# Kernel tuning notes

Measured on AMD Instinct MI355X. Metric: run time of the kernel, lower is better.

Reference implementation:

```python
import jax, jax.numpy as jnp
import numpy as np

K = 9          # kernel_size
PAD = K // 2   # 'same' padding, stride 1
SIGMA = 1.0
EPS = 1e-5     # BatchNorm eps

def _windows(a):
    # a: (B, C, L) -> (B, C, K, L); zero-padded sliding windows (== F.unfold semantics)
    L = a.shape[-1]
    ap = jnp.pad(a, ((0, 0), (0, 0), (PAD, PAD)))
    return jnp.stack([ap[:, :, k:k + L] for k in range(K)], axis=2)

def setup_inputs() -> dict:
    key = jax.random.key(0)
    ks = jax.random.split(key, 4)
    B, Cin, Cout, L = 8, 256, 256, 16384
    x = jax.random.normal(ks[0], (B, Cin, L), jnp.float32)
    coords = jax.random.uniform(ks[1], (B, 3, L), jnp.float32)
    conv_w = jax.random.normal(ks[2], (Cout, Cin, K), jnp.float32) * np.float32(1.0 / np.sqrt(Cin * K))
    conv_b = jnp.zeros((Cout,), jnp.float32)
    gamma = jnp.ones((Cout,), jnp.float32)
    beta = jnp.zeros((Cout,), jnp.float32)
    return {"x": x, "coords": coords, "conv_w": conv_w, "conv_b": conv_b, "gamma": gamma, "beta": beta}

def reference(x, coords, conv_w, conv_b, gamma, beta):
    # --- WeightedConv1D: Gaussian coordinate weights on each unfolded window element ---
    cw = _windows(coords)                                      # (B, 3, K, L)
    d2 = jnp.sum((cw - coords[:, :, None, :]) ** 2, axis=1)    # (B, K, L) squared dist to window center
    w = jnp.exp(-d2 / (2.0 * SIGMA ** 2))                      # (B, K, L) Gaussian weights
    xw = _windows(x) * w[:, None, :, :]                        # (B, Cin, K, L) weighted windows
    y = jnp.einsum('bckl,ock->bol', xw, conv_w) + conv_b[None, :, None]  # (B, Cout, L)
    # --- BatchNorm1d (training-mode batch statistics, biased variance) + ReLU ---
    mu = jnp.mean(y, axis=(0, 2), keepdims=True)
    var = jnp.var(y, axis=(0, 2), keepdims=True)
    yhat = (y - mu) * jax.lax.rsqrt(var + EPS)
    out = jax.nn.relu(yhat * gamma[None, :, None] + beta[None, :, None])
    # Dropout with drop=0.0 is the identity.
    return out
```

## Files before the change

kernel.cpp:

```cpp
#include <hip/hip_runtime.h>
#include <hip/hip_bf16.h>


typedef float        f32x4  __attribute__((ext_vector_type(4)));
typedef short        bf16x8 __attribute__((ext_vector_type(8)));
typedef unsigned int u32x4  __attribute__((ext_vector_type(4)));

#define LLEN 16384

__device__ __forceinline__ unsigned short bf16bits(float a) {
  return __builtin_bit_cast(unsigned short, __float2bfloat16(a));
}
__device__ __forceinline__ unsigned packbf(float a, float b) {
  return (unsigned)bf16bits(a) | ((unsigned)bf16bits(b) << 16);
}

__global__ void k_prep(const float* __restrict__ cw,
                       unsigned short* __restrict__ Aperm,
                       float* __restrict__ sums) {
  const int idx = blockIdx.x * 256 + threadIdx.x;
  if (idx < 512) sums[idx] = 0.0f;
  const int o   = idx / 2304;
  const int rem = idx - o * 2304;
  const int c   = rem / 9;
  const int kk  = rem - c * 9;
  Aperm[((size_t)kk * 256 + o) * 256 + c] = bf16bits(cw[idx]);
}

__global__ void k_w(const float* __restrict__ coords, float* __restrict__ wbuf) {
  const int gidx = blockIdx.x * 256 + threadIdx.x;
  const int b = gidx >> 14, l = gidx & (LLEN - 1);
  const float* cb = coords + (size_t)b * 3 * LLEN;
  const float c0 = cb[l], c1 = cb[LLEN + l], c2v = cb[2 * LLEN + l];
#pragma unroll
  for (int kk = 0; kk < 9; ++kk) {
    const int lc = l + kk - 4;
    float a0 = 0.f, a1 = 0.f, a2 = 0.f;
    if (lc >= 0 && lc < LLEN) { a0 = cb[lc]; a1 = cb[LLEN + lc]; a2 = cb[2 * LLEN + lc]; }
    const float d0 = a0 - c0, d1 = a1 - c1, d2 = a2 - c2v;
    wbuf[(((size_t)(b * 9 + kk)) << 14) + l] = __expf(-0.5f * (d0 * d0 + d1 * d1 + d2 * d2));
  }
}

__global__ __launch_bounds__(512, 2) void k_gemm(
    const float* __restrict__ x, const float* __restrict__ wbuf,
    const unsigned short* __restrict__ Aperm, const float* __restrict__ convb,
    float* __restrict__ y, float* __restrict__ sums) {
  __shared__ __align__(16) unsigned short Ash[256][72];
  __shared__ __align__(16) unsigned short Xsh[264][72];

  const int tid  = threadIdx.x;
  const int lane = tid & 63, wv = tid >> 6;
  const int wm = wv >> 2, wn = wv & 3;
  const int hi = lane >> 4, lo16 = lane & 15;
  const int b  = blockIdx.x >> 6, lt = blockIdx.x & 63;
  const int l0 = lt << 8;

  f32x4 acc[8][4];
#pragma unroll
  for (int i = 0; i < 8; ++i)
#pragma unroll
    for (int j = 0; j < 4; ++j) acc[i][j] = f32x4{0.f, 0.f, 0.f, 0.f};

  const int arow  = tid >> 3;
  const int acol8 = (tid & 7) * 8;
  const int nbase = wn * 64 + lo16;

  u32x4 ar[4];
  float wl[4], wln[4];

#pragma unroll
  for (int p = 0; p < 4; ++p)
    ar[p] = *reinterpret_cast<const u32x4*>(
        Aperm + ((size_t)(p * 64 + arow)) * 256 + acol8);
#pragma unroll
  for (int nt = 0; nt < 4; ++nt)
    wl[nt] = wbuf[((size_t)(b * 9) << 14) + l0 + nbase + nt * 16];

#pragma unroll 1
  for (int cc = 0; cc < 4; ++cc) {
    __syncthreads();
    {
      const int c = tid >> 3, rg = tid & 7;
      const float* xrow = x + ((size_t)(b * 256 + cc * 64 + c)) * LLEN;
#pragma unroll 1
      for (int grp = rg; grp < 66; grp += 8) {
        const int lx = l0 - 4 + grp * 4;
        f32x4 v;
        if (lx >= 0 && lx <= LLEN - 4) {
          v = *reinterpret_cast<const f32x4*>(xrow + lx);
        } else {
#pragma unroll
          for (int q = 0; q < 4; ++q) {
            const int lq = lx + q;
            v[q] = (lq >= 0 && lq < LLEN) ? xrow[lq] : 0.f;
          }
        }
#pragma unroll
        for (int q = 0; q < 4; ++q) Xsh[grp * 4 + q][c] = bf16bits(v[q]);
      }
    }
#pragma unroll 1
    for (int kk = 0; kk < 9; ++kk) {
      if (kk) __syncthreads();
#pragma unroll
      for (int p = 0; p < 4; ++p)
        *reinterpret_cast<u32x4*>(reinterpret_cast<char*>(&Ash[0][0]) +
                                  (p * 64 + arow) * 144 + acol8 * 2) = ar[p];
      int nkk = kk + 1, ncc = cc;
      if (nkk == 9) { nkk = 0; ++ncc; if (ncc == 4) { ncc = 3; nkk = 8; } }
#pragma unroll
      for (int p = 0; p < 4; ++p)
        ar[p] = *reinterpret_cast<const u32x4*>(
            Aperm + ((size_t)nkk * 256 + p * 64 + arow) * 256 + ncc * 64 + acol8);
#pragma unroll
      for (int nt = 0; nt < 4; ++nt)
        wln[nt] = wbuf[((size_t)(b * 9 + nkk) << 14) + l0 + nbase + nt * 16];
      __syncthreads();
#pragma unroll
      for (int kb = 0; kb < 2; ++kb) {
        bf16x8 bfrag[4];
#pragma unroll
        for (int nt = 0; nt < 4; ++nt) {
          const int r = nbase + nt * 16 + kk;
          const u32x4 xr = *reinterpret_cast<const u32x4*>(
              reinterpret_cast<const char*>(&Xsh[0][0]) + r * 144 + kb * 64 + hi * 16);
          const float wv2 = wl[nt];
          u32x4 o4;
#pragma unroll
          for (int q = 0; q < 4; ++q) {
            const unsigned u = xr[q];
            const float flo = __builtin_bit_cast(float, u << 16) * wv2;
            const float fhi = __builtin_bit_cast(float, u & 0xffff0000u) * wv2;
            o4[q] = packbf(flo, fhi);
          }
          bfrag[nt] = __builtin_bit_cast(bf16x8, o4);
        }
#pragma unroll
        for (int mt = 0; mt < 8; ++mt) {
          const int orow = wm * 128 + mt * 16 + lo16;
          const bf16x8 af = *reinterpret_cast<const bf16x8*>(
              reinterpret_cast<const char*>(&Ash[0][0]) + orow * 144 + kb * 64 + hi * 16);
#pragma unroll
          for (int nt = 0; nt < 4; ++nt)
            acc[mt][nt] = __builtin_amdgcn_mfma_f32_16x16x32_bf16(af, bfrag[nt],
                                                                  acc[mt][nt], 0, 0, 0);
        }
      }
#pragma unroll
      for (int nt = 0; nt < 4; ++nt) wl[nt] = wln[nt];
    }
  }

  __syncthreads();
  float* red = reinterpret_cast<float*>(&Ash[0][0]);
  red[tid] = 0.0f;
  __syncthreads();
#pragma unroll
  for (int mt = 0; mt < 8; ++mt) {
#pragma unroll
    for (int v = 0; v < 4; ++v) {
      const int o = wm * 128 + mt * 16 + hi * 4 + v;
      const float cb = convb[o];
      float s = 0.f, s2 = 0.f;
#pragma unroll
      for (int nt = 0; nt < 4; ++nt) {
        const int l = l0 + nbase + nt * 16;
        const float yv = acc[mt][nt][v] + cb;
        y[(((size_t)b * 256 + o) << 14) + l] = yv;
        s += yv; s2 += yv * yv;
      }
#pragma unroll
      for (int d = 1; d < 16; d <<= 1) { s += __shfl_xor(s, d); s2 += __shfl_xor(s2, d); }
      if (lo16 == 0) { atomicAdd(&red[o], s); atomicAdd(&red[o + 256], s2); }
    }
  }
  __syncthreads();
  atomicAdd(&sums[tid], red[tid]);
}

__global__ void k_norm(float* __restrict__ y, const float* __restrict__ sums,
                       const float* __restrict__ gamma, const float* __restrict__ beta) {
  const size_t i0 = ((size_t)blockIdx.x * 256 + threadIdx.x) * 8;
  const int o = (int)((i0 >> 14) & 255);
  const float n = 131072.f;
  const float mu = sums[o] / n;
  float var = sums[256 + o] / n - mu * mu;
  var = fmaxf(var, 0.f);
  const float sc = rsqrtf(var + 1e-5f) * gamma[o];
  const float bb = beta[o] - mu * sc;
  f32x4 v0 = *reinterpret_cast<const f32x4*>(y + i0);
  f32x4 v1 = *reinterpret_cast<const f32x4*>(y + i0 + 4);
#pragma unroll
  for (int i = 0; i < 4; ++i) {
    v0[i] = fmaxf(v0[i] * sc + bb, 0.f);
    v1[i] = fmaxf(v1[i] * sc + bb, 0.f);
  }
  *reinterpret_cast<f32x4*>(y + i0) = v0;
  *reinterpret_cast<f32x4*>(y + i0 + 4) = v1;
}

extern "C" void kernel_launch(void* const* d_in, const int* in_sizes, int n_in,
                              void* d_out, int out_size, void* d_ws, size_t ws_size,
                              hipStream_t stream) {
  const float* x      = (const float*)d_in[0];
  const float* coords = (const float*)d_in[1];
  const float* conv_w = (const float*)d_in[2];
  const float* conv_b = (const float*)d_in[3];
  const float* gamma  = (const float*)d_in[4];
  const float* beta   = (const float*)d_in[5];
  float* out = (float*)d_out;

  float* sums = (float*)d_ws;
  float* wbuf = (float*)((char*)d_ws + 4096);
  unsigned short* Aperm =
      (unsigned short*)((char*)d_ws + 4096 + (size_t)8 * 9 * LLEN * 4);

  k_prep<<<2304, 256, 0, stream>>>(conv_w, Aperm, sums);
  k_w<<<512, 256, 0, stream>>>(coords, wbuf);
  k_gemm<<<512, 512, 0, stream>>>(x, wbuf, Aperm, conv_b, out, sums);
  k_norm<<<16384, 256, 0, stream>>>(out, sums, gamma, beta);
}
```

Before: 273.5 us.

## Load GEMM weight fragments directly from global memory and prefetch x chunks in registers

Drops the shared-memory staging of the conv-weight tile, so each wave reads its A fragments straight from the permuted bf16 weight buffer in global memory (L2-resident). This removes the per-tap A store and two syncs per inner iteration. The next x channel chunk is prefetched into registers as packed bf16 while the current chunk is computed. Float-to-bf16 packing now uses the hardware v_cvt_pk_bf16_f32 instruction. In exchange it adds redundant global and L2 traffic for weights across waves, with load latency exposed inside the MFMA loop, plus more register pressure.

```diff
diff --git a/kernel.cpp b/kernel.cpp
--- a/kernel.cpp
+++ b/kernel.cpp
@@ -4,6 +4,7 @@
 
 typedef float        f32x4  __attribute__((ext_vector_type(4)));
 typedef short        bf16x8 __attribute__((ext_vector_type(8)));
+typedef unsigned int u32x2  __attribute__((ext_vector_type(2)));
 typedef unsigned int u32x4  __attribute__((ext_vector_type(4)));
 
 #define LLEN 16384
@@ -11,8 +12,10 @@
 __device__ __forceinline__ unsigned short bf16bits(float a) {
   return __builtin_bit_cast(unsigned short, __float2bfloat16(a));
 }
-__device__ __forceinline__ unsigned packbf(float a, float b) {
-  return (unsigned)bf16bits(a) | ((unsigned)bf16bits(b) << 16);
+__device__ __forceinline__ unsigned cvt_pk_bf16(float lo, float hi) {
+  unsigned r;
+  asm("v_cvt_pk_bf16_f32 %0, %1, %2" : "=v"(r) : "v"(lo), "v"(hi));
+  return r;
 }
 
 __global__ void k_prep(const float* __restrict__ cw,
@@ -46,7 +49,6 @@
     const float* __restrict__ x, const float* __restrict__ wbuf,
     const unsigned short* __restrict__ Aperm, const float* __restrict__ convb,
     float* __restrict__ y, float* __restrict__ sums) {
-  __shared__ __align__(16) unsigned short Ash[256][72];
   __shared__ __align__(16) unsigned short Xsh[264][72];
 
   const int tid  = threadIdx.x;
@@ -55,6 +57,7 @@
   const int hi = lane >> 4, lo16 = lane & 15;
   const int b  = blockIdx.x >> 6, lt = blockIdx.x & 63;
   const int l0 = lt << 8;
+  const int nbase = wn * 64 + lo16;
 
   f32x4 acc[8][4];
 #pragma unroll
@@ -62,98 +65,89 @@
 #pragma unroll
     for (int j = 0; j < 4; ++j) acc[i][j] = f32x4{0.f, 0.f, 0.f, 0.f};
 
-  const int arow  = tid >> 3;
-  const int acol8 = (tid & 7) * 8;
-  const int nbase = wn * 64 + lo16;
-
-  u32x4 ar[4];
-  float wl[4], wln[4];
-
-#pragma unroll
-  for (int p = 0; p < 4; ++p)
-    ar[p] = *reinterpret_cast<const u32x4*>(
-        Aperm + ((size_t)(p * 64 + arow)) * 256 + acol8);
-#pragma unroll
-  for (int nt = 0; nt < 4; ++nt)
-    wl[nt] = wbuf[((size_t)(b * 9) << 14) + l0 + nbase + nt * 16];
-
+  const int c = tid >> 3, rg = tid & 7;
+  u32x2 xp[9];
+
+  auto loadx = [&](int cc) {
+    const float* xrow = x + ((size_t)(b * 256 + cc * 64 + c)) * LLEN;
+#pragma unroll
+    for (int i = 0; i < 9; ++i) {
+      const int grp = rg + 8 * i;
+      f32x4 v = {0.f, 0.f, 0.f, 0.f};
+      const int lx = l0 - 4 + grp * 4;
+      if (grp < 66 && lx >= 0 && lx <= LLEN - 4)
+        v = *reinterpret_cast<const f32x4*>(xrow + lx);
+      xp[i][0] = cvt_pk_bf16(v[0], v[1]);
+      xp[i][1] = cvt_pk_bf16(v[2], v[3]);
+    }
+  };
+  auto storex = [&]() {
+#pragma unroll
+    for (int i = 0; i < 9; ++i) {
+      const int grp = rg + 8 * i;
+      if (grp < 66) {
+        const int r = grp * 4;
+        Xsh[r + 0][c] = (unsigned short)(xp[i][0] & 0xffffu);
+        Xsh[r + 1][c] = (unsigned short)(xp[i][0] >> 16);
+        Xsh[r + 2][c] = (unsigned short)(xp[i][1] & 0xffffu);
+        Xsh[r + 3][c] = (unsigned short)(xp[i][1] >> 16);
+      }
+    }
+  };
+
+  loadx(0);
 #pragma unroll 1
   for (int cc = 0; cc < 4; ++cc) {
+    if (cc) __syncthreads();
+    storex();
     __syncthreads();
-    {
-      const int c = tid >> 3, rg = tid & 7;
-      const float* xrow = x + ((size_t)(b * 256 + cc * 64 + c)) * LLEN;
-#pragma unroll 1
-      for (int grp = rg; grp < 66; grp += 8) {
-        const int lx = l0 - 4 + grp * 4;
-        f32x4 v;
-        if (lx >= 0 && lx <= LLEN - 4) {
-          v = *reinterpret_cast<const f32x4*>(xrow + lx);
-        } else {
-#pragma unroll
-          for (int q = 0; q < 4; ++q) {
-            const int lq = lx + q;
-            v[q] = (lq >= 0 && lq < LLEN) ? xrow[lq] : 0.f;
-          }
-        }
-#pragma unroll
-        for (int q = 0; q < 4; ++q) Xsh[grp * 4 + q][c] = bf16bits(v[q]);
-      }
-    }
+    if (cc < 3) loadx(cc + 1);
+
 #pragma unroll 1
     for (int kk = 0; kk < 9; ++kk) {
-      if (kk) __syncthreads();
-#pragma unroll
-      for (int p = 0; p < 4; ++p)
-        *reinterpret_cast<u32x4*>(reinterpret_cast<char*>(&Ash[0][0]) +
-                                  (p * 64 + arow) * 144 + acol8 * 2) = ar[p];
-      int nkk = kk + 1, ncc = cc;
-      if (nkk == 9) { nkk = 0; ++ncc; if (ncc == 4) { ncc = 3; nkk = 8; } }
-#pragma unroll
-      for (int p = 0; p < 4; ++p)
-        ar[p] = *reinterpret_cast<const u32x4*>(
-            Aperm + ((size_t)nkk * 256 + p * 64 + arow) * 256 + ncc * 64 + acol8);
+      float wl[4];
 #pragma unroll
       for (int nt = 0; nt < 4; ++nt)
-        wln[nt] = wbuf[((size_t)(b * 9 + nkk) << 14) + l0 + nbase + nt * 16];
-      __syncthreads();
+        wl[nt] = wbuf[((size_t)(b * 9 + kk) << 14) + l0 + nbase + nt * 16];
+      const unsigned short* Abase =
+          Aperm + ((size_t)kk * 256 + wm * 128 + lo16) * 256 + cc * 64 + hi * 8;
+
 #pragma unroll
       for (int kb = 0; kb < 2; ++kb) {
-        bf16x8 bfrag[4];
+        u32x4 ag[8];
+#pragma unroll
+        for (int mt = 0; mt < 8; ++mt)
+          ag[mt] = *reinterpret_cast<const u32x4*>(Abase + mt * 16 * 256 + kb * 32);
+        bf16x8 bf[4];
 #pragma unroll
         for (int nt = 0; nt < 4; ++nt) {
           const int r = nbase + nt * 16 + kk;
-          const u32x4 xr = *reinterpret_cast<const u32x4*>(
+          const u32x4 xv = *reinterpret_cast<const u32x4*>(
               reinterpret_cast<const char*>(&Xsh[0][0]) + r * 144 + kb * 64 + hi * 16);
           const float wv2 = wl[nt];
           u32x4 o4;
 #pragma unroll
           for (int q = 0; q < 4; ++q) {
-            const unsigned u = xr[q];
-            const float flo = __builtin_bit_cast(float, u << 16) * wv2;
-            const float fhi = __builtin_bit_cast(float, u & 0xffff0000u) * wv2;
-            o4[q] = packbf(flo, fhi);
+            const float flo = __builtin_bit_cast(float, xv[q] << 16) * wv2;
+            const float fhi = __builtin_bit_cast(float, xv[q] & 0xffff0000u) * wv2;
+            o4[q] = cvt_pk_bf16(flo, fhi);
           }
-          bfrag[nt] = __builtin_bit_cast(bf16x8, o4);
+          bf[nt] = __builtin_bit_cast(bf16x8, o4);
         }
 #pragma unroll
         for (int mt = 0; mt < 8; ++mt) {
-          const int orow = wm * 128 + mt * 16 + lo16;
-          const bf16x8 af = *reinterpret_cast<const bf16x8*>(
-              reinterpret_cast<const char*>(&Ash[0][0]) + orow * 144 + kb * 64 + hi * 16);
+          const bf16x8 af = __builtin_bit_cast(bf16x8, ag[mt]);
 #pragma unroll
           for (int nt = 0; nt < 4; ++nt)
-            acc[mt][nt] = __builtin_amdgcn_mfma_f32_16x16x32_bf16(af, bfrag[nt],
+            acc[mt][nt] = __builtin_amdgcn_mfma_f32_16x16x32_bf16(af, bf[nt],
                                                                   acc[mt][nt], 0, 0, 0);
         }
       }
-#pragma unroll
-      for (int nt = 0; nt < 4; ++nt) wl[nt] = wln[nt];
     }
   }
 
   __syncthreads();
-  float* red = reinterpret_cast<float*>(&Ash[0][0]);
+  float* red = reinterpret_cast<float*>(&Xsh[0][0]);
   red[tid] = 0.0f;
   __syncthreads();
 #pragma unroll
```

New measurement: 389.1 us. 42.3% more time.
